# Kernel tuning notes

Measured on AMD Instinct MI355X. Metric: run time of the kernel, lower is better.

Reference implementation:

```python
import jax, jax.numpy as jnp
import numpy as np

N, C, H, W = 8, 3, 720, 1280


def setup_inputs() -> dict:
    key = jax.random.key(0)
    k1, k2 = jax.random.split(key)
    image = jax.random.normal(k1, (N, C, H, W), dtype=jnp.float32)
    # scale flow so integer truncation gives real displacements (and collisions)
    flow = jax.random.normal(k2, (N, 2, H, W), dtype=jnp.float32) * 20.0
    return {"image": image, "flow": flow}


def _warp_fw(image, flow):
    n, c, h, w = image.shape
    hw = h * w
    # flat source mesh coordinates (same for all batches)
    mx = jnp.broadcast_to(jnp.arange(w, dtype=jnp.int32)[None, :], (h, w)).reshape(-1)
    my = jnp.broadcast_to(jnp.arange(h, dtype=jnp.int32)[:, None], (h, w)).reshape(-1)
    fx = flow[:, 0].reshape(n, hw)
    fy = flow[:, 1].reshape(n, hw)
    # torch .long() truncates toward zero; astype(int32) matches
    wx = jnp.clip(mx[None, :] + fx.astype(jnp.int32), 0, w - 1)
    wy = jnp.clip(my[None, :] + fy.astype(jnp.int32), 0, h - 1)
    tgt = wy * w + wx  # (n, hw) linear target index
    v = fx * fx + fy * fy
    sortidx = jnp.argsort(v, axis=1)  # (n, hw) ascending
    ranks = jnp.arange(hw, dtype=jnp.int32)

    def per_batch(sortidx_i, tgt_i):
        # rank[p] = position of source pixel p in the sorted write order
        rank = jnp.zeros((hw,), jnp.int32).at[sortidx_i].set(ranks)
        # winning (max) rank at each target location; -1 = hole
        best = jnp.full((hw,), -1, jnp.int32).at[tgt_i].max(rank)
        covered = best >= 0
        # winning source pixel index = sortidx[best_rank]
        src = jnp.take(sortidx_i, jnp.clip(best, 0, hw - 1))
        return src, covered

    src, covered = jax.vmap(per_batch)(sortidx, tgt)  # (n, hw) each
    img_flat = image.reshape(n, c, hw)
    gathered = jnp.take_along_axis(
        img_flat, jnp.broadcast_to(src[:, None, :], (n, c, hw)), axis=2
    )
    out = jnp.where(covered[:, None, :], gathered, 0.0)
    return out.reshape(n, c, h, w)


def reference(image, flow):
    return _warp_fw(image, flow)
```

## Files before the change

### kernel.cpp

```cpp
#include <hip/hip_runtime.h>
#include <cstdint>

constexpr int N_ = 8;
constexpr int C_ = 3;
constexpr int H_ = 720;
constexpr int W_ = 1280;
constexpr int HW = H_ * W_;

constexpr int TW = 128;
constexpr int TH = 64;
constexpr int M_ = 64;
constexpr int NTX = W_ / TW;
constexpr int NTY = (H_ + TH - 1) / TH;
constexpr int BLK = 1024;
constexpr int OSEG = 16384;
constexpr int SCAP = 128;
constexpr int CSTRIDE = 16;
constexpr int BPB = HW / 1024;

typedef float vf4 __attribute__((ext_vector_type(4)));

struct Outlier { unsigned long long key; int tgt; int pad; };

__device__ __forceinline__ unsigned long long make_key(float fx, float fy, int p) {
    float v = __fadd_rn(__fmul_rn(fx, fx), __fmul_rn(fy, fy));
    return ((unsigned long long)__float_as_uint(v) << 32) | (unsigned int)(p + 1);
}

__global__ __launch_bounds__(256) void outlier_kernel(
    const float* __restrict__ flow,
    unsigned long long* __restrict__ ocnt,
    Outlier* __restrict__ olist) {
    __shared__ unsigned int bcnt;
    __shared__ unsigned long long gbase;
    __shared__ unsigned long long skey[SCAP];
    __shared__ int stgt[SCAP];
    if (threadIdx.x == 0) bcnt = 0;
    __syncthreads();

    int n  = blockIdx.x / BPB;
    int p0 = (blockIdx.x - n * BPB) * 1024 + threadIdx.x * 4;
    const float* f = flow + (size_t)n * 2 * HW;
    vf4 fx4 = *(const vf4*)(f + p0);
    vf4 fy4 = *(const vf4*)(f + HW + p0);
    float fxs[4] = {fx4.x, fx4.y, fx4.z, fx4.w};
    float fys[4] = {fy4.x, fy4.y, fy4.z, fy4.w};
    int y = p0 / W_;
    int x0 = p0 - y * W_;
    #pragma unroll
    for (int i = 0; i < 4; ++i) {
        int dx = (int)fxs[i];
        int dy = (int)fys[i];
        if (dx > M_ || dx < -M_ || dy > M_ || dy < -M_) {
            int wx = min(max(x0 + i + dx, 0), W_ - 1);
            int wy = min(max(y + dy, 0), H_ - 1);
            unsigned long long key = make_key(fxs[i], fys[i], p0 + i);
            int tgt = wy * W_ + wx;
            unsigned int s = atomicAdd(&bcnt, 1u);
            if (s < (unsigned)SCAP) {
                skey[s] = key; stgt[s] = tgt;
            } else {
                unsigned long long o = atomicAdd(&ocnt[(size_t)n * CSTRIDE], 1ULL);
                if (o < (unsigned long long)OSEG) {
                    Outlier e; e.key = key; e.tgt = tgt; e.pad = 0;
                    olist[n * OSEG + (int)o] = e;
                }
            }
        }
    }
    __syncthreads();
    unsigned int c = bcnt > (unsigned)SCAP ? (unsigned)SCAP : bcnt;
    if (threadIdx.x == 0)
        gbase = c ? atomicAdd(&ocnt[(size_t)n * CSTRIDE], (unsigned long long)c)
                  : 0ULL;
    __syncthreads();
    for (unsigned int i = threadIdx.x; i < c; i += 256) {
        unsigned long long o = gbase + i;
        if (o < (unsigned long long)OSEG) {
            Outlier e; e.key = skey[i]; e.tgt = stgt[i]; e.pad = 0;
            olist[n * OSEG + (int)o] = e;
        }
    }
}

__global__ __launch_bounds__(BLK, 8) void warp_tile_kernel(
    const float* __restrict__ image,
    const float* __restrict__ flow,
    const unsigned long long* __restrict__ ocnt,
    const Outlier* __restrict__ olist,
    float* __restrict__ out) {
    __shared__ unsigned long long lkey[TH * TW];
    int bid = blockIdx.x;
    int n    = bid & 7;
    int tile = bid >> 3;
    int tyi = tile / NTX;
    int txi = tile - tyi * NTX;
    int tx0 = txi * TW;
    int ty0 = tyi * TH;
    int th_eff = min(TH, H_ - ty0);
    int tid = threadIdx.x;

    for (int i = tid; i < TH * TW; i += BLK) lkey[i] = 0ULL;
    __syncthreads();

    int wy0 = max(0, ty0 - M_), wy1 = min(H_, ty0 + th_eff + M_);
    int wx0 = max(0, tx0 - M_), wx1 = min(W_, tx0 + TW + M_);
    const float* fx_p = flow + (size_t)n * 2 * HW;
    const float* fy_p = fx_p + HW;

    int x4   = wx0 + ((tid & 63) << 2);
    int rowg = tid >> 6;
    if (x4 < wx1) {
        #pragma unroll 2
        for (int y = wy0 + rowg; y < wy1; y += 16) {
            int pbase = y * W_ + x4;
            vf4 fx4 = *(const vf4*)(fx_p + pbase);
            vf4 fy4 = *(const vf4*)(fy_p + pbase);
            float fxs[4] = {fx4.x, fx4.y, fx4.z, fx4.w};
            float fys[4] = {fy4.x, fy4.y, fy4.z, fy4.w};
            #pragma unroll
            for (int i = 0; i < 4; ++i) {
                float fx = fxs[i], fy = fys[i];
                int wx = x4 + i + (int)fx;
                int wy = y + (int)fy;
                wx = min(max(wx, 0), W_ - 1);
                wy = min(max(wy, 0), H_ - 1);
                int lx = wx - tx0, ly = wy - ty0;
                if ((unsigned)lx < (unsigned)TW && (unsigned)ly < (unsigned)th_eff) {
                    atomicMax(&lkey[ly * TW + lx], make_key(fx, fy, pbase + i));
                }
            }
        }
    }
    __syncthreads();

    unsigned long long craw = ocnt[(size_t)n * CSTRIDE];
    int cnt = (int)(craw > (unsigned long long)OSEG ? OSEG : craw);
    const Outlier* seg = olist + n * OSEG;
    for (int o = tid; o < cnt; o += BLK) {
        Outlier e = seg[o];
        int ey = e.tgt / W_, ex = e.tgt - ey * W_;
        int lx = ex - tx0, ly = ey - ty0;
        if ((unsigned)lx < (unsigned)TW && (unsigned)ly < (unsigned)th_eff)
            atomicMax(&lkey[ly * TW + lx], e.key);
    }
    __syncthreads();

    const float* img_n = image + (size_t)n * C_ * HW;
    float* out_n = out + (size_t)n * C_ * HW;
    int q4 = th_eff * (TW / 4);
    for (int s = tid; s < q4; s += BLK) {
        int r = s >> 5;
        int cg = s & 31;
        int lp = r * TW + cg * 4;
        unsigned long long k0 = lkey[lp],     k1 = lkey[lp + 1];
        unsigned long long k2 = lkey[lp + 2], k3 = lkey[lp + 3];
        int s0 = (int)(unsigned int)(k0 & 0xffffffffULL) - 1;
        int s1 = (int)(unsigned int)(k1 & 0xffffffffULL) - 1;
        int s2 = (int)(unsigned int)(k2 & 0xffffffffULL) - 1;
        int s3 = (int)(unsigned int)(k3 & 0xffffffffULL) - 1;
        int op = (ty0 + r) * W_ + tx0 + cg * 4;
        #pragma unroll
        for (int c = 0; c < C_; ++c) {
            const float* pl = img_n + (size_t)c * HW;
            vf4 o;
            o.x = k0 ? pl[s0] : 0.0f;
            o.y = k1 ? pl[s1] : 0.0f;
            o.z = k2 ? pl[s2] : 0.0f;
            o.w = k3 ? pl[s3] : 0.0f;
            __builtin_nontemporal_store(o, (vf4*)(out_n + (size_t)c * HW + op));
        }
    }
}

extern "C" void kernel_launch(void* const* d_in, const int* in_sizes, int n_in,
                              void* d_out, int out_size, void* d_ws, size_t ws_size,
                              hipStream_t stream) {
    const float* image = (const float*)d_in[0];
    const float* flow  = (const float*)d_in[1];
    float* out = (float*)d_out;

    unsigned long long* ocnt = (unsigned long long*)d_ws;
    Outlier* olist = (Outlier*)((char*)d_ws + 1024);

    (void)hipMemsetAsync(ocnt, 0, 1024, stream);

    int k0_blocks = (N_ * HW / 4) / 256;
    outlier_kernel<<<k0_blocks, 256, 0, stream>>>(flow, ocnt, olist);

    warp_tile_kernel<<<N_ * NTX * NTY, BLK, 0, stream>>>(
        image, flow, ocnt, olist, out);
}
```

Baseline: 288.6 us.

## Make warp tile kernel persistent with per-batch atomic tile queue

Replaces the one-block-per-tile grid with a fixed grid of persistent blocks that fetch tile indices from a per-batch atomic counter in workspace. LDS key clearing is vectorised with 128-bit stores. This aims to cut block launch overhead and balance work across CUs. In exchange, each tile adds an atomic and a barrier, and the fixed block-to-batch split may leave load imbalance at the tail.

```diff
diff --git a/kernel.cpp b/kernel.cpp
--- a/kernel.cpp
+++ b/kernel.cpp
@@ -12,7 +12,9 @@
 constexpr int M_ = 64;
 constexpr int NTX = W_ / TW;
 constexpr int NTY = (H_ + TH - 1) / TH;
+constexpr int NTILES = NTX * NTY;
 constexpr int BLK = 1024;
+constexpr int PBLK = 512;
 constexpr int OSEG = 16384;
 constexpr int SCAP = 128;
 constexpr int CSTRIDE = 16;
@@ -87,88 +89,103 @@
     const float* __restrict__ image,
     const float* __restrict__ flow,
     const unsigned long long* __restrict__ ocnt,
+    unsigned int* __restrict__ tctr,
     const Outlier* __restrict__ olist,
     float* __restrict__ out) {
     __shared__ unsigned long long lkey[TH * TW];
-    int bid = blockIdx.x;
-    int n    = bid & 7;
-    int tile = bid >> 3;
-    int tyi = tile / NTX;
-    int txi = tile - tyi * NTX;
-    int tx0 = txi * TW;
-    int ty0 = tyi * TH;
-    int th_eff = min(TH, H_ - ty0);
+    __shared__ int s_tile;
+    int n   = blockIdx.x & 7;
     int tid = threadIdx.x;
 
-    for (int i = tid; i < TH * TW; i += BLK) lkey[i] = 0ULL;
-    __syncthreads();
-
-    int wy0 = max(0, ty0 - M_), wy1 = min(H_, ty0 + th_eff + M_);
-    int wx0 = max(0, tx0 - M_), wx1 = min(W_, tx0 + TW + M_);
     const float* fx_p = flow + (size_t)n * 2 * HW;
     const float* fy_p = fx_p + HW;
-
-    int x4   = wx0 + ((tid & 63) << 2);
-    int rowg = tid >> 6;
-    if (x4 < wx1) {
-        #pragma unroll 2
-        for (int y = wy0 + rowg; y < wy1; y += 16) {
-            int pbase = y * W_ + x4;
-            vf4 fx4 = *(const vf4*)(fx_p + pbase);
-            vf4 fy4 = *(const vf4*)(fy_p + pbase);
-            float fxs[4] = {fx4.x, fx4.y, fx4.z, fx4.w};
-            float fys[4] = {fy4.x, fy4.y, fy4.z, fy4.w};
-            #pragma unroll
-            for (int i = 0; i < 4; ++i) {
-                float fx = fxs[i], fy = fys[i];
-                int wx = x4 + i + (int)fx;
-                int wy = y + (int)fy;
-                wx = min(max(wx, 0), W_ - 1);
-                wy = min(max(wy, 0), H_ - 1);
-                int lx = wx - tx0, ly = wy - ty0;
-                if ((unsigned)lx < (unsigned)TW && (unsigned)ly < (unsigned)th_eff) {
-                    atomicMax(&lkey[ly * TW + lx], make_key(fx, fy, pbase + i));
-                }
-            }
-        }
-    }
-    __syncthreads();
-
+    const float* img_n = image + (size_t)n * C_ * HW;
+    float* out_n = out + (size_t)n * C_ * HW;
     unsigned long long craw = ocnt[(size_t)n * CSTRIDE];
     int cnt = (int)(craw > (unsigned long long)OSEG ? OSEG : craw);
     const Outlier* seg = olist + n * OSEG;
-    for (int o = tid; o < cnt; o += BLK) {
-        Outlier e = seg[o];
-        int ey = e.tgt / W_, ex = e.tgt - ey * W_;
-        int lx = ex - tx0, ly = ey - ty0;
-        if ((unsigned)lx < (unsigned)TW && (unsigned)ly < (unsigned)th_eff)
-            atomicMax(&lkey[ly * TW + lx], e.key);
-    }
-    __syncthreads();
-
-    const float* img_n = image + (size_t)n * C_ * HW;
-    float* out_n = out + (size_t)n * C_ * HW;
-    int q4 = th_eff * (TW / 4);
-    for (int s = tid; s < q4; s += BLK) {
-        int r = s >> 5;
-        int cg = s & 31;
-        int lp = r * TW + cg * 4;
-        unsigned long long k0 = lkey[lp],     k1 = lkey[lp + 1];
-        unsigned long long k2 = lkey[lp + 2], k3 = lkey[lp + 3];
-        int s0 = (int)(unsigned int)(k0 & 0xffffffffULL) - 1;
-        int s1 = (int)(unsigned int)(k1 & 0xffffffffULL) - 1;
-        int s2 = (int)(unsigned int)(k2 & 0xffffffffULL) - 1;
-        int s3 = (int)(unsigned int)(k3 & 0xffffffffULL) - 1;
-        int op = (ty0 + r) * W_ + tx0 + cg * 4;
-        #pragma unroll
-        for (int c = 0; c < C_; ++c) {
-            const float* pl = img_n + (size_t)c * HW;
-            vf4 o;
-            o.x = k0 ? pl[s0] : 0.0f;
-            o.y = k1 ? pl[s1] : 0.0f;
-            o.z = k2 ? pl[s2] : 0.0f;
-            o.w = k3 ? pl[s3] : 0.0f;
-            __builtin_nontemporal_store(o, (vf4*)(out_n + (size_t)c * HW + op));
+    unsigned int* my_ctr = tctr + (size_t)n * 32;
+
+    for (;;) {
+        if (tid == 0) s_tile = (int)atomicAdd(my_ctr, 1u);
+        __syncthreads();
+        int tile = s_tile;
+        if (tile >= NTILES) break;
+        int tyi = tile / NTX;
+        int txi = tile - tyi * NTX;
+        int tx0 = txi * TW;
+        int ty0 = tyi * TH;
+        int th_eff = min(TH, H_ - ty0);
+
+        {
+            ulonglong2 z; z.x = 0ULL; z.y = 0ULL;
+            ulonglong2* l2p = (ulonglong2*)lkey;
+            #pragma unroll
+            for (int i = 0; i < (TH * TW) / 2 / BLK; ++i)
+                l2p[tid + i * BLK] = z;
+        }
+        __syncthreads();
+
+        int wy0 = max(0, ty0 - M_), wy1 = min(H_, ty0 + th_eff + M_);
+        int wx0 = max(0, tx0 - M_), wx1 = min(W_, tx0 + TW + M_);
+        int x4   = wx0 + ((tid & 63) << 2);
+        int rowg = tid >> 6;
+        if (x4 < wx1) {
+            #pragma unroll 2
+            for (int y = wy0 + rowg; y < wy1; y += 16) {
+                int pbase = y * W_ + x4;
+                vf4 fx4 = *(const vf4*)(fx_p + pbase);
+                vf4 fy4 = *(const vf4*)(fy_p + pbase);
+                float fxs[4] = {fx4.x, fx4.y, fx4.z, fx4.w};
+                float fys[4] = {fy4.x, fy4.y, fy4.z, fy4.w};
+                #pragma unroll
+                for (int i = 0; i < 4; ++i) {
+                    float fx = fxs[i], fy = fys[i];
+                    int wx = x4 + i + (int)fx;
+                    int wy = y + (int)fy;
+                    wx = min(max(wx, 0), W_ - 1);
+                    wy = min(max(wy, 0), H_ - 1);
+                    int lx = wx - tx0, ly = wy - ty0;
+                    if ((unsigned)lx < (unsigned)TW &&
+                        (unsigned)ly < (unsigned)th_eff) {
+                        atomicMax(&lkey[ly * TW + lx], make_key(fx, fy, pbase + i));
+                    }
+                }
+            }
+        }
+        __syncthreads();
+
+        for (int o = tid; o < cnt; o += BLK) {
+            Outlier e = seg[o];
+            int ey = e.tgt / W_, ex = e.tgt - ey * W_;
+            int lx = ex - tx0, ly = ey - ty0;
+            if ((unsigned)lx < (unsigned)TW && (unsigned)ly < (unsigned)th_eff)
+                atomicMax(&lkey[ly * TW + lx], e.key);
+        }
+        __syncthreads();
+
+        int q4 = th_eff * (TW / 4);
+        for (int s = tid; s < q4; s += BLK) {
+            int r = s >> 5;
+            int cg = s & 31;
+            int lp = r * TW + cg * 4;
+            unsigned long long k0 = lkey[lp],     k1 = lkey[lp + 1];
+            unsigned long long k2 = lkey[lp + 2], k3 = lkey[lp + 3];
+            int s0 = (int)(unsigned int)(k0 & 0xffffffffULL) - 1;
+            int s1 = (int)(unsigned int)(k1 & 0xffffffffULL) - 1;
+            int s2 = (int)(unsigned int)(k2 & 0xffffffffULL) - 1;
+            int s3 = (int)(unsigned int)(k3 & 0xffffffffULL) - 1;
+            int op = (ty0 + r) * W_ + tx0 + cg * 4;
+            #pragma unroll
+            for (int c = 0; c < C_; ++c) {
+                const float* pl = img_n + (size_t)c * HW;
+                vf4 o;
+                o.x = k0 ? pl[s0] : 0.0f;
+                o.y = k1 ? pl[s1] : 0.0f;
+                o.z = k2 ? pl[s2] : 0.0f;
+                o.w = k3 ? pl[s3] : 0.0f;
+                __builtin_nontemporal_store(o, (vf4*)(out_n + (size_t)c * HW + op));
+            }
         }
     }
 }
@@ -181,13 +198,14 @@
     float* out = (float*)d_out;
 
     unsigned long long* ocnt = (unsigned long long*)d_ws;
-    Outlier* olist = (Outlier*)((char*)d_ws + 1024);
-
-    (void)hipMemsetAsync(ocnt, 0, 1024, stream);
+    unsigned int* tctr = (unsigned int*)((char*)d_ws + 1024);
+    Outlier* olist = (Outlier*)((char*)d_ws + 2048);
+
+    (void)hipMemsetAsync(d_ws, 0, 2048, stream);
 
     int k0_blocks = (N_ * HW / 4) / 256;
     outlier_kernel<<<k0_blocks, 256, 0, stream>>>(flow, ocnt, olist);
 
-    warp_tile_kernel<<<N_ * NTX * NTY, BLK, 0, stream>>>(
-        image, flow, ocnt, olist, out);
-}
+    warp_tile_kernel<<<PBLK, BLK, 0, stream>>>(
+        image, flow, ocnt, tctr, olist, out);
+}
```

Result: slower. 305.2 us (+5.8%).
